# Kernel tuning notes

Measured on AMD Instinct MI355X. Metric: run time of the kernel, lower is better.

## Reference

```python
import jax, jax.numpy as jnp
import numpy as np

OUT, N_GROUPS, GROUP = 11008, 32, 128
IN = N_GROUPS * GROUP  # 4096
RANK = 128
B, S = 1, 64


def setup_inputs() -> dict:
    key = jax.random.key(0)
    ks = jax.random.split(key, 7)
    x = jax.random.normal(ks[0], (B, S, IN), dtype=jnp.float32)
    weight = jax.random.randint(ks[1], (OUT, N_GROUPS, GROUP), 0, 16, dtype=jnp.int32)
    scale = jax.random.uniform(ks[2], (OUT, N_GROUPS), dtype=jnp.float32) * 0.02 + 1e-3
    zero_point = jax.random.uniform(ks[3], (OUT, N_GROUPS), dtype=jnp.float32) * 15.0
    svd_up = jax.random.normal(ks[4], (OUT, RANK), dtype=jnp.float32) * 0.02
    svd_down = jax.random.normal(ks[5], (RANK, IN), dtype=jnp.float32) * 0.02
    bias = jax.random.normal(ks[6], (OUT,), dtype=jnp.float32) * 0.01
    return {"x": x, "weight": weight, "scale": scale, "zero_point": zero_point,
            "svd_up": svd_up, "svd_down": svd_down, "bias": bias}


def _dequantize(weight, scale, zero_point, svd_up, svd_down):
    # group-wise dequant: (W_q - zp) * scale, per (out, group) pair
    W = (weight.astype(jnp.float32) - zero_point[:, :, None]) * scale[:, :, None]
    W = W.reshape(weight.shape[0], -1)  # [OUT, IN]
    # low-rank SVD correction
    return W + svd_up @ svd_down


def reference(x, weight, scale, zero_point, svd_up, svd_down, bias):
    # int8 dynamic-quant path (token count 64 >= 16, int8_matmul=True)
    xt = x.reshape(-1, x.shape[-1])                       # [T, IN]
    W_f = _dequantize(weight, scale, zero_point, svd_up, svd_down).T  # [IN, OUT]
    scale_x = jnp.max(jnp.abs(xt), axis=1, keepdims=True) / 127.0     # [T, 1]
    x_q = jnp.clip(jnp.round(xt / scale_x), -128, 127).astype(jnp.int8)
    scale_w = jnp.max(jnp.abs(W_f), axis=0, keepdims=True) / 127.0    # [1, OUT]
    W_q8 = jnp.clip(jnp.round(W_f / scale_w), -128, 127).astype(jnp.int8)
    acc = jnp.matmul(x_q, W_q8, preferred_element_type=jnp.int32)     # [T, OUT] int32
    out = acc.astype(jnp.float32) * scale_x * scale_w
    return out[None] + bias  # [1, T, OUT], matching torch's unsqueeze(0) + bias
```

## Files before the change

kernel.cpp:

```cpp
#include <hip/hip_runtime.h>
#include <string.h>

#define OUT_DIM 11008
#define IN_DIM  4096
#define NTOK    64
#define RANK    128
#define NG      32

typedef float        v4f  __attribute__((ext_vector_type(4)));
typedef int          v4i  __attribute__((ext_vector_type(4)));
typedef unsigned int v4u  __attribute__((ext_vector_type(4)));
typedef _Float16     v8h  __attribute__((ext_vector_type(8)));

__device__ inline unsigned int pack2h(float lo, float hi) {
  union { _Float16 h[2]; unsigned int u; } t;
  t.h[0] = (_Float16)lo; t.h[1] = (_Float16)hi;
  return t.u;
}

__global__ __launch_bounds__(256) void pack_d_kernel(const float* __restrict__ d,
                                                     unsigned int* __restrict__ dp) {
  int idx = (blockIdx.x * 256 + threadIdx.x) * 4;
  int r2 = idx >> 12, c = idx & 4095;
  v4f a = *(const v4f*)(d + (2 * r2) * IN_DIM + c);
  v4f b = *(const v4f*)(d + (2 * r2 + 1) * IN_DIM + c);
  v4u o;
#pragma unroll
  for (int e = 0; e < 4; e++) o[e] = pack2h(a[e], b[e]);
  *(v4u*)(dp + idx) = o;
}

__global__ __launch_bounds__(256) void quant_x_kernel(const float* __restrict__ x,
                                                      signed char* __restrict__ xq,
                                                      float* __restrict__ sx) {
  int t = blockIdx.x, tid = threadIdx.x;
  const float* row = x + t * IN_DIM;
  v4f v[4];
  float m = 0.f;
#pragma unroll
  for (int i = 0; i < 4; i++) {
    v[i] = *(const v4f*)(row + tid * 16 + i * 4);
#pragma unroll
    for (int e = 0; e < 4; e++) m = fmaxf(m, fabsf(v[i][e]));
  }
#pragma unroll
  for (int off = 1; off < 64; off <<= 1) m = fmaxf(m, __shfl_xor(m, off));
  __shared__ float wm[4];
  if ((tid & 63) == 0) wm[tid >> 6] = m;
  __syncthreads();
  m = fmaxf(fmaxf(wm[0], wm[1]), fmaxf(wm[2], wm[3]));
  float s = m / 127.0f;
  if (tid == 0) sx[t] = s;
  unsigned int packed[4];
#pragma unroll
  for (int i = 0; i < 4; i++) {
    int q[4];
#pragma unroll
    for (int e = 0; e < 4; e++) {
      float qf = rintf(v[i][e] / s);
      qf = fminf(127.f, fmaxf(-128.f, qf));
      q[e] = (int)qf;
    }
    packed[i] = (q[0] & 255) | ((q[1] & 255) << 8) | ((q[2] & 255) << 16) | ((q[3] & 255) << 24);
  }
  *(v4u*)(xq + t * IN_DIM + tid * 16) = *(v4u*)packed;
}

__device__ inline void load_u(const float* __restrict__ svd_up, _Float16 (*U)[136],
                              int tid, int r0) {
#pragma unroll
  for (int i = 0; i < 16; i++) {
    int idx = i * 256 + tid;
    int r = idx >> 7, k = idx & 127;
    U[r][k] = (_Float16)svd_up[(r0 + r) * RANK + k];
  }
}

__device__ inline void stage_d(const unsigned int* __restrict__ dp, unsigned int (*Dl)[128],
                               int tid, int kt) {
  int c = (tid & 31) * 4;
#pragma unroll
  for (int i = 0; i < 8; i++) {
    int r2 = i * 8 + (tid >> 5);
    *(v4u*)&Dl[r2][c] = *(const v4u*)(dp + r2 * IN_DIM + kt * 128 + c);
  }
}

__device__ inline void svd_mfma(const _Float16 (*U)[136], const unsigned int (*Dl)[128],
                                int l, int w, v4f acc[2][2]) {
#pragma unroll
  for (int ks = 0; ks < 4; ks++) {
    v8h a0 = *(const v8h*)&U[(l & 15)][ks * 32 + (l >> 4) * 8];
    v8h a1 = *(const v8h*)&U[16 + (l & 15)][ks * 32 + (l >> 4) * 8];
#pragma unroll
    for (int fn = 0; fn < 2; fn++) {
      int col = w * 32 + fn * 16 + (l & 15);
      int rb = ks * 16 + (l >> 4) * 4;
      union { unsigned int u[4]; v8h h; } bu;
      bu.u[0] = Dl[rb][col];
      bu.u[1] = Dl[rb + 1][col];
      bu.u[2] = Dl[rb + 2][col];
      bu.u[3] = Dl[rb + 3][col];
      acc[0][fn] = __builtin_amdgcn_mfma_f32_16x16x32_f16(a0, bu.h, acc[0][fn], 0, 0, 0);
      acc[1][fn] = __builtin_amdgcn_mfma_f32_16x16x32_f16(a1, bu.h, acc[1][fn], 0, 0, 0);
    }
  }
}

__global__ __launch_bounds__(256, 2) void rowmax_kernel(const int* __restrict__ wq,
    const float* __restrict__ scale, const float* __restrict__ zp,
    const float* __restrict__ svd_up, const unsigned int* __restrict__ dp,
    float* __restrict__ sw) {
  __shared__ _Float16 U[32][136];
  __shared__ unsigned int Dl[64][128];
  __shared__ float Cl[32][132];
  int tid = threadIdx.x;
  int r0 = blockIdx.x * 32;
  load_u(svd_up, U, tid, r0);
  int l = tid & 63, w = tid >> 6;
  int myrow = tid >> 3, c0 = (tid & 7) * 16;
  float rmax = 0.f;
  __syncthreads();
  for (int kt = 0; kt < 32; kt++) {
    stage_d(dp, Dl, tid, kt);
    __syncthreads();
    v4f acc[2][2] = {};
    svd_mfma(U, Dl, l, w, acc);
#pragma unroll
    for (int fm = 0; fm < 2; fm++)
#pragma unroll
      for (int fn = 0; fn < 2; fn++)
#pragma unroll
        for (int j = 0; j < 4; j++)
          Cl[fm * 16 + (l >> 4) * 4 + j][w * 32 + fn * 16 + (l & 15)] = acc[fm][fn][j];
    __syncthreads();
    float s = scale[(r0 + myrow) * NG + kt];
    float z = zp[(r0 + myrow) * NG + kt];
    const v4i* wp = (const v4i*)(wq + (r0 + myrow) * IN_DIM + kt * 128 + c0);
#pragma unroll
    for (int i = 0; i < 4; i++) {
      v4i wv = wp[i];
      v4f cv = *(const v4f*)&Cl[myrow][c0 + i * 4];
#pragma unroll
      for (int e = 0; e < 4; e++) {
        float W = ((float)wv[e] - z) * s + cv[e];
        rmax = fmaxf(rmax, fabsf(W));
      }
    }
    __syncthreads();
  }
  rmax = fmaxf(rmax, __shfl_xor(rmax, 1));
  rmax = fmaxf(rmax, __shfl_xor(rmax, 2));
  rmax = fmaxf(rmax, __shfl_xor(rmax, 4));
  if ((tid & 7) == 0) sw[r0 + myrow] = rmax / 127.0f;
}

__global__ __launch_bounds__(256, 2) void matmul_kernel(const int* __restrict__ wq,
    const float* __restrict__ scale, const float* __restrict__ zp,
    const float* __restrict__ svd_up, const unsigned int* __restrict__ dp,
    const signed char* __restrict__ xq, const float* __restrict__ sx,
    const float* __restrict__ sw, const float* __restrict__ bias,
    float* __restrict__ out) {
  __shared__ _Float16 U[32][136];
  __shared__ unsigned int Dl[64][128];
  __shared__ float Cl[32][132];
  __shared__ unsigned int W8[32][33];
  __shared__ float sxl[64];
  int tid = threadIdx.x;
  int r0 = blockIdx.x * 32;
  load_u(svd_up, U, tid, r0);
  if (tid < 64) sxl[tid] = sx[tid];
  int l = tid & 63, w = tid >> 6;
  int myrow = tid >> 3, c0 = (tid & 7) * 16;
  float swr = sw[r0 + myrow];
  v4i oacc[2] = {};
  __syncthreads();
  for (int kt = 0; kt < 32; kt++) {
    stage_d(dp, Dl, tid, kt);
    __syncthreads();
    v4f acc[2][2] = {};
    svd_mfma(U, Dl, l, w, acc);
#pragma unroll
    for (int fm = 0; fm < 2; fm++)
#pragma unroll
      for (int fn = 0; fn < 2; fn++)
#pragma unroll
        for (int j = 0; j < 4; j++)
          Cl[fm * 16 + (l >> 4) * 4 + j][w * 32 + fn * 16 + (l & 15)] = acc[fm][fn][j];
    __syncthreads();
    float s = scale[(r0 + myrow) * NG + kt];
    float z = zp[(r0 + myrow) * NG + kt];
    const v4i* wp = (const v4i*)(wq + (r0 + myrow) * IN_DIM + kt * 128 + c0);
#pragma unroll
    for (int i = 0; i < 4; i++) {
      v4i wv = wp[i];
      v4f cv = *(const v4f*)&Cl[myrow][c0 + i * 4];
      int q[4];
#pragma unroll
      for (int e = 0; e < 4; e++) {
        float W = ((float)wv[e] - z) * s + cv[e];
        float qf = rintf(W / swr);
        qf = fminf(127.f, fmaxf(-128.f, qf));
        q[e] = (int)qf;
      }
      W8[myrow][(c0 >> 2) + i] =
          (q[0] & 255) | ((q[1] & 255) << 8) | ((q[2] & 255) << 16) | ((q[3] & 255) << 24);
    }
    __syncthreads();
#pragma unroll
    for (int ks = 0; ks < 2; ks++) {
      v4i a = *(const v4i*)(xq + (w * 16 + (l & 15)) * IN_DIM + kt * 128 + ks * 64 + (l >> 4) * 16);
#pragma unroll
      for (int fr = 0; fr < 2; fr++) {
        int rr = fr * 16 + (l & 15);
        int kd = ks * 16 + (l >> 4) * 4;
        v4i b;
        b[0] = (int)W8[rr][kd];
        b[1] = (int)W8[rr][kd + 1];
        b[2] = (int)W8[rr][kd + 2];
        b[3] = (int)W8[rr][kd + 3];
        oacc[fr] = __builtin_amdgcn_mfma_i32_16x16x64_i8(a, b, oacc[fr], 0, 0, 0);
      }
    }
  }
#pragma unroll
  for (int fr = 0; fr < 2; fr++) {
#pragma unroll
    for (int j = 0; j < 4; j++) {
      int token = w * 16 + (l >> 4) * 4 + j;
      int orow = r0 + fr * 16 + (l & 15);
      float v = (float)oacc[fr][j] * sxl[token] * sw[orow] + bias[orow];
      out[token * OUT_DIM + orow] = v;
    }
  }
}

extern "C" void kernel_launch(void* const* d_in, const int* in_sizes, int n_in,
                              void* d_out, int out_size, void* d_ws, size_t ws_size,
                              hipStream_t stream) {
  (void)in_sizes; (void)n_in; (void)out_size; (void)ws_size;
  const float* x        = (const float*)d_in[0];
  const int*   wq       = (const int*)d_in[1];
  const float* scale    = (const float*)d_in[2];
  const float* zp       = (const float*)d_in[3];
  const float* svd_up   = (const float*)d_in[4];
  const float* svd_down = (const float*)d_in[5];
  const float* bias     = (const float*)d_in[6];
  float* out = (float*)d_out;

  char* ws = (char*)d_ws;
  unsigned int* dp = (unsigned int*)ws;
  signed char*  xq = (signed char*)(ws + 1048576);
  float*        sx = (float*)(ws + 1048576 + 262144);
  float*        sw = (float*)(ws + 1048576 + 262144 + 256);

  pack_d_kernel<<<256, 256, 0, stream>>>(svd_down, dp);
  quant_x_kernel<<<NTOK, 256, 0, stream>>>(x, xq, sx);
  rowmax_kernel<<<OUT_DIM / 32, 256, 0, stream>>>(wq, scale, zp, svd_up, dp, sw);
  matmul_kernel<<<OUT_DIM / 32, 256, 0, stream>>>(wq, scale, zp, svd_up, dp, xq, sx, sw, bias, out);
}
```

Baseline: 390.3 us.

## Materialize SVD correction once, pack int4 weights, split-K matmul with atomics

```diff
diff --git a/kernel.cpp b/kernel.cpp
--- a/kernel.cpp
+++ b/kernel.cpp
@@ -10,6 +10,7 @@
 typedef float        v4f  __attribute__((ext_vector_type(4)));
 typedef int          v4i  __attribute__((ext_vector_type(4)));
 typedef unsigned int v4u  __attribute__((ext_vector_type(4)));
+typedef unsigned int v2u  __attribute__((ext_vector_type(2)));
 typedef _Float16     v8h  __attribute__((ext_vector_type(8)));
 
 __device__ inline unsigned int pack2h(float lo, float hi) {
@@ -28,42 +29,6 @@
 #pragma unroll
   for (int e = 0; e < 4; e++) o[e] = pack2h(a[e], b[e]);
   *(v4u*)(dp + idx) = o;
-}
-
-__global__ __launch_bounds__(256) void quant_x_kernel(const float* __restrict__ x,
-                                                      signed char* __restrict__ xq,
-                                                      float* __restrict__ sx) {
-  int t = blockIdx.x, tid = threadIdx.x;
-  const float* row = x + t * IN_DIM;
-  v4f v[4];
-  float m = 0.f;
-#pragma unroll
-  for (int i = 0; i < 4; i++) {
-    v[i] = *(const v4f*)(row + tid * 16 + i * 4);
-#pragma unroll
-    for (int e = 0; e < 4; e++) m = fmaxf(m, fabsf(v[i][e]));
-  }
-#pragma unroll
-  for (int off = 1; off < 64; off <<= 1) m = fmaxf(m, __shfl_xor(m, off));
-  __shared__ float wm[4];
-  if ((tid & 63) == 0) wm[tid >> 6] = m;
-  __syncthreads();
-  m = fmaxf(fmaxf(wm[0], wm[1]), fmaxf(wm[2], wm[3]));
-  float s = m / 127.0f;
-  if (tid == 0) sx[t] = s;
-  unsigned int packed[4];
-#pragma unroll
-  for (int i = 0; i < 4; i++) {
-    int q[4];
-#pragma unroll
-    for (int e = 0; e < 4; e++) {
-      float qf = rintf(v[i][e] / s);
-      qf = fminf(127.f, fmaxf(-128.f, qf));
-      q[e] = (int)qf;
-    }
-    packed[i] = (q[0] & 255) | ((q[1] & 255) << 8) | ((q[2] & 255) << 16) | ((q[3] & 255) << 24);
-  }
-  *(v4u*)(xq + t * IN_DIM + tid * 16) = *(v4u*)packed;
 }
 
 __device__ inline void load_u(const float* __restrict__ svd_up, _Float16 (*U)[136],
@@ -107,22 +72,18 @@
   }
 }
 
-__global__ __launch_bounds__(256, 2) void rowmax_kernel(const int* __restrict__ wq,
-    const float* __restrict__ scale, const float* __restrict__ zp,
-    const float* __restrict__ svd_up, const unsigned int* __restrict__ dp,
-    float* __restrict__ sw) {
+__global__ __launch_bounds__(256) void cgemm_kernel(const float* __restrict__ svd_up,
+    const unsigned int* __restrict__ dp, _Float16* __restrict__ Cb) {
   __shared__ _Float16 U[32][136];
   __shared__ unsigned int Dl[64][128];
-  __shared__ float Cl[32][132];
   int tid = threadIdx.x;
   int r0 = blockIdx.x * 32;
   load_u(svd_up, U, tid, r0);
   int l = tid & 63, w = tid >> 6;
-  int myrow = tid >> 3, c0 = (tid & 7) * 16;
-  float rmax = 0.f;
   __syncthreads();
-  for (int kt = 0; kt < 32; kt++) {
-    stage_d(dp, Dl, tid, kt);
+  for (int ct = 0; ct < 4; ct++) {
+    int ktile = blockIdx.y * 4 + ct;
+    stage_d(dp, Dl, tid, ktile);
     __syncthreads();
     v4f acc[2][2] = {};
     svd_mfma(U, Dl, l, w, acc);
@@ -131,85 +92,132 @@
 #pragma unroll
       for (int fn = 0; fn < 2; fn++)
 #pragma unroll
-        for (int j = 0; j < 4; j++)
-          Cl[fm * 16 + (l >> 4) * 4 + j][w * 32 + fn * 16 + (l & 15)] = acc[fm][fn][j];
-    __syncthreads();
-    float s = scale[(r0 + myrow) * NG + kt];
-    float z = zp[(r0 + myrow) * NG + kt];
-    const v4i* wp = (const v4i*)(wq + (r0 + myrow) * IN_DIM + kt * 128 + c0);
-#pragma unroll
-    for (int i = 0; i < 4; i++) {
-      v4i wv = wp[i];
-      v4f cv = *(const v4f*)&Cl[myrow][c0 + i * 4];
-#pragma unroll
-      for (int e = 0; e < 4; e++) {
-        float W = ((float)wv[e] - z) * s + cv[e];
-        rmax = fmaxf(rmax, fabsf(W));
-      }
-    }
-    __syncthreads();
-  }
-  rmax = fmaxf(rmax, __shfl_xor(rmax, 1));
-  rmax = fmaxf(rmax, __shfl_xor(rmax, 2));
-  rmax = fmaxf(rmax, __shfl_xor(rmax, 4));
-  if ((tid & 7) == 0) sw[r0 + myrow] = rmax / 127.0f;
-}
-
-__global__ __launch_bounds__(256, 2) void matmul_kernel(const int* __restrict__ wq,
+        for (int j = 0; j < 4; j++) {
+          int row = r0 + fm * 16 + (l >> 4) * 4 + j;
+          int col = ktile * 128 + w * 32 + fn * 16 + (l & 15);
+          Cb[row * IN_DIM + col] = (_Float16)acc[fm][fn][j];
+        }
+    __syncthreads();
+  }
+}
+
+__global__ __launch_bounds__(256) void rowmax_kernel(const int* __restrict__ wq,
     const float* __restrict__ scale, const float* __restrict__ zp,
-    const float* __restrict__ svd_up, const unsigned int* __restrict__ dp,
-    const signed char* __restrict__ xq, const float* __restrict__ sx,
-    const float* __restrict__ sw, const float* __restrict__ bias,
-    float* __restrict__ out) {
-  __shared__ _Float16 U[32][136];
-  __shared__ unsigned int Dl[64][128];
-  __shared__ float Cl[32][132];
+    const _Float16* __restrict__ Cb, unsigned int* __restrict__ wpk,
+    float* __restrict__ swmax) {
+  int tid = threadIdx.x;
+  int lane = tid & 63, w = tid >> 6;
+  int r = blockIdx.x * 4 + w;
+  const int* wrow = wq + r * IN_DIM;
+  const _Float16* crow = Cb + r * IN_DIM;
+  unsigned int* prow = wpk + r * (IN_DIM / 8);
+  const float* srow = scale + r * NG;
+  const float* zrow = zp + r * NG;
+  float m = 0.f;
+  for (int j = 0; j < 8; j++) {
+    int d = j * 64 + lane;
+    int e0 = d * 8;
+    v4i w0 = *(const v4i*)(wrow + e0);
+    v4i w1 = *(const v4i*)(wrow + e0 + 4);
+    union { v4u u; _Float16 h[8]; } cc;
+    cc.u = *(const v4u*)(crow + e0);
+    int g = e0 >> 7;
+    float s = srow[g], z = zrow[g];
+    unsigned int o = (unsigned)(w0[0] & 15)         | ((unsigned)(w0[1] & 15) << 4)
+                   | ((unsigned)(w0[2] & 15) << 8)  | ((unsigned)(w0[3] & 15) << 12)
+                   | ((unsigned)(w1[0] & 15) << 16) | ((unsigned)(w1[1] & 15) << 20)
+                   | ((unsigned)(w1[2] & 15) << 24) | ((unsigned)(w1[3] & 15) << 28);
+    prow[d] = o;
+#pragma unroll
+    for (int k = 0; k < 4; k++) {
+      m = fmaxf(m, fabsf(((float)w0[k] - z) * s + (float)cc.h[k]));
+      m = fmaxf(m, fabsf(((float)w1[k] - z) * s + (float)cc.h[k + 4]));
+    }
+  }
+#pragma unroll
+  for (int off = 1; off < 64; off <<= 1) m = fmaxf(m, __shfl_xor(m, off));
+  if (lane == 0) swmax[r] = m;
+}
+
+__global__ __launch_bounds__(256) void quant_x_kernel(const float* __restrict__ x,
+                                                      signed char* __restrict__ xq,
+                                                      float* __restrict__ sx) {
+  int t = blockIdx.x, tid = threadIdx.x;
+  const float* row = x + t * IN_DIM;
+  v4f v[4];
+  float m = 0.f;
+#pragma unroll
+  for (int i = 0; i < 4; i++) {
+    v[i] = *(const v4f*)(row + tid * 16 + i * 4);
+#pragma unroll
+    for (int e = 0; e < 4; e++) m = fmaxf(m, fabsf(v[i][e]));
+  }
+#pragma unroll
+  for (int off = 1; off < 64; off <<= 1) m = fmaxf(m, __shfl_xor(m, off));
+  __shared__ float wm[4];
+  if ((tid & 63) == 0) wm[tid >> 6] = m;
+  __syncthreads();
+  m = fmaxf(fmaxf(wm[0], wm[1]), fmaxf(wm[2], wm[3]));
+  float s = m / 127.0f;
+  if (tid == 0) sx[t] = s;
+  unsigned int packed[4];
+#pragma unroll
+  for (int i = 0; i < 4; i++) {
+    int q[4];
+#pragma unroll
+    for (int e = 0; e < 4; e++) {
+      float qf = rintf(v[i][e] / s);
+      qf = fminf(127.f, fmaxf(-128.f, qf));
+      q[e] = (int)qf;
+    }
+    packed[i] = (q[0] & 255) | ((q[1] & 255) << 8) | ((q[2] & 255) << 16) | ((q[3] & 255) << 24);
+  }
+  *(v4u*)(xq + t * IN_DIM + tid * 16) = *(v4u*)packed;
+}
+
+__global__ __launch_bounds__(256) void matmul_kernel(const unsigned int* __restrict__ wpk,
+    const float* __restrict__ scale, const float* __restrict__ zp,
+    const _Float16* __restrict__ Cb, const signed char* __restrict__ xq,
+    const float* __restrict__ swmax, int* __restrict__ acc32) {
   __shared__ unsigned int W8[32][33];
-  __shared__ float sxl[64];
   int tid = threadIdx.x;
   int r0 = blockIdx.x * 32;
-  load_u(svd_up, U, tid, r0);
-  if (tid < 64) sxl[tid] = sx[tid];
+  int kc = blockIdx.y;
   int l = tid & 63, w = tid >> 6;
   int myrow = tid >> 3, c0 = (tid & 7) * 16;
-  float swr = sw[r0 + myrow];
+  float swr = swmax[r0 + myrow] / 127.0f;
   v4i oacc[2] = {};
-  __syncthreads();
-  for (int kt = 0; kt < 32; kt++) {
-    stage_d(dp, Dl, tid, kt);
-    __syncthreads();
-    v4f acc[2][2] = {};
-    svd_mfma(U, Dl, l, w, acc);
-#pragma unroll
-    for (int fm = 0; fm < 2; fm++)
-#pragma unroll
-      for (int fn = 0; fn < 2; fn++)
-#pragma unroll
-        for (int j = 0; j < 4; j++)
-          Cl[fm * 16 + (l >> 4) * 4 + j][w * 32 + fn * 16 + (l & 15)] = acc[fm][fn][j];
-    __syncthreads();
-    float s = scale[(r0 + myrow) * NG + kt];
-    float z = zp[(r0 + myrow) * NG + kt];
-    const v4i* wp = (const v4i*)(wq + (r0 + myrow) * IN_DIM + kt * 128 + c0);
+  for (int kt = 0; kt < 8; kt++) {
+    int kbase = kc * 1024 + kt * 128;
+    int g = kbase >> 7;
+    float s = scale[(r0 + myrow) * NG + g];
+    float z = zp[(r0 + myrow) * NG + g];
+    v2u pk = *(const v2u*)(wpk + (r0 + myrow) * (IN_DIM / 8) + ((kbase + c0) >> 3));
+    union { v4u u[2]; _Float16 h[16]; } cc;
+    cc.u[0] = *(const v4u*)(Cb + (r0 + myrow) * IN_DIM + kbase + c0);
+    cc.u[1] = *(const v4u*)(Cb + (r0 + myrow) * IN_DIM + kbase + c0 + 8);
+    unsigned int wd[4];
 #pragma unroll
     for (int i = 0; i < 4; i++) {
-      v4i wv = wp[i];
-      v4f cv = *(const v4f*)&Cl[myrow][c0 + i * 4];
       int q[4];
 #pragma unroll
       for (int e = 0; e < 4; e++) {
-        float W = ((float)wv[e] - z) * s + cv[e];
+        int jj = i * 4 + e;
+        int qn = (pk[jj >> 3] >> (4 * (jj & 7))) & 15;
+        float W = ((float)qn - z) * s + (float)cc.h[jj];
         float qf = rintf(W / swr);
         qf = fminf(127.f, fmaxf(-128.f, qf));
         q[e] = (int)qf;
       }
-      W8[myrow][(c0 >> 2) + i] =
-          (q[0] & 255) | ((q[1] & 255) << 8) | ((q[2] & 255) << 16) | ((q[3] & 255) << 24);
-    }
+      wd[i] = (q[0] & 255) | ((q[1] & 255) << 8) | ((q[2] & 255) << 16) | ((q[3] & 255) << 24);
+    }
+    __syncthreads();
+#pragma unroll
+    for (int i = 0; i < 4; i++) W8[myrow][(c0 >> 2) + i] = wd[i];
     __syncthreads();
 #pragma unroll
     for (int ks = 0; ks < 2; ks++) {
-      v4i a = *(const v4i*)(xq + (w * 16 + (l & 15)) * IN_DIM + kt * 128 + ks * 64 + (l >> 4) * 16);
+      v4i a = *(const v4i*)(xq + (w * 16 + (l & 15)) * IN_DIM + kbase + ks * 64 + (l >> 4) * 16);
 #pragma unroll
       for (int fr = 0; fr < 2; fr++) {
         int rr = fr * 16 + (l & 15);
@@ -224,15 +232,22 @@
     }
   }
 #pragma unroll
-  for (int fr = 0; fr < 2; fr++) {
+  for (int fr = 0; fr < 2; fr++)
 #pragma unroll
     for (int j = 0; j < 4; j++) {
       int token = w * 16 + (l >> 4) * 4 + j;
       int orow = r0 + fr * 16 + (l & 15);
-      float v = (float)oacc[fr][j] * sxl[token] * sw[orow] + bias[orow];
-      out[token * OUT_DIM + orow] = v;
-    }
-  }
+      atomicAdd(acc32 + token * OUT_DIM + orow, oacc[fr][j]);
+    }
+}
+
+__global__ __launch_bounds__(256) void epilogue_kernel(const int* __restrict__ acc32,
+    const float* __restrict__ sx, const float* __restrict__ swmax,
+    const float* __restrict__ bias, float* __restrict__ out) {
+  int o = blockIdx.x * 256 + threadIdx.x;
+  int t = blockIdx.y;
+  float swv = swmax[o] / 127.0f;
+  out[t * OUT_DIM + o] = (float)acc32[t * OUT_DIM + o] * sx[t] * swv + bias[o];
 }
 
 extern "C" void kernel_launch(void* const* d_in, const int* in_sizes, int n_in,
@@ -249,13 +264,19 @@
   float* out = (float*)d_out;
 
   char* ws = (char*)d_ws;
-  unsigned int* dp = (unsigned int*)ws;
-  signed char*  xq = (signed char*)(ws + 1048576);
-  float*        sx = (float*)(ws + 1048576 + 262144);
-  float*        sw = (float*)(ws + 1048576 + 262144 + 256);
+  unsigned int* dp    = (unsigned int*)(ws);
+  signed char*  xq    = (signed char*)(ws + 1048576);
+  float*        sx    = (float*)(ws + 1310720);
+  float*        swmax = (float*)(ws + 1310976);
+  unsigned int* wpk   = (unsigned int*)(ws + 1355008);
+  _Float16*     Cb    = (_Float16*)(ws + 23899392);
+  int*          acc32 = (int*)(ws + 114076928);
 
   pack_d_kernel<<<256, 256, 0, stream>>>(svd_down, dp);
+  cgemm_kernel<<<dim3(OUT_DIM / 32, 8), 256, 0, stream>>>(svd_up, dp, Cb);
+  rowmax_kernel<<<OUT_DIM / 4, 256, 0, stream>>>(wq, scale, zp, Cb, wpk, swmax);
   quant_x_kernel<<<NTOK, 256, 0, stream>>>(x, xq, sx);
-  rowmax_kernel<<<OUT_DIM / 32, 256, 0, stream>>>(wq, scale, zp, svd_up, dp, sw);
-  matmul_kernel<<<OUT_DIM / 32, 256, 0, stream>>>(wq, scale, zp, svd_up, dp, xq, sx, sw, bias, out);
-}
+  hipMemsetAsync(acc32, 0, NTOK * OUT_DIM * sizeof(int), stream);
+  matmul_kernel<<<dim3(OUT_DIM / 32, 4), 256, 0, stream>>>(wpk, scale, zp, Cb, xq, swmax, acc32);
+  epilogue_kernel<<<dim3(OUT_DIM / 256, NTOK), 256, 0, stream>>>(acc32, sx, swmax, bias, out);
+}
```

After: 352.7 us. 1.11x faster.
